# Optimization experiments

Hardware: AMD Instinct MI355X
Metric: run time of the kernel (lower is better)

## Reference

```python
import jax, jax.numpy as jnp
from jax import lax
import numpy as np

B, C, H, W = 64, 3, 224, 224
NPARAM, NSEV, NCHROMA, K = 8, 5, 1, 37
SEVERITY = 3  # ctor default
CHROMA = 0   # random.random()*nchroma made deterministic


def setup_inputs() -> dict:
    key = jax.random.key(0)
    k1, k2, k3, k4, k5 = jax.random.split(key, 5)
    batch = jax.random.uniform(k1, (B, C, H, W), dtype=jnp.float32)
    targets = jax.random.randint(k2, (B,), 0, 1000, dtype=jnp.int32)
    psf_stack = jax.random.uniform(k3, (NPARAM, NSEV, NCHROMA, C, K, K), dtype=jnp.float32)
    params = jax.random.randint(k4, (B,), 0, NPARAM, dtype=jnp.int32)
    weights = jax.random.uniform(k5, (B,), dtype=jnp.float32)
    return {"batch": batch, "targets": targets, "psf_stack": psf_stack,
            "params": params, "weights": weights}


def reference(batch, targets, psf_stack, params, weights):
    # kernels for chosen severity/chroma: [NPARAM, C, K, K]
    kernels = psf_stack[:, SEVERITY - 1, CHROMA]
    k = kernels[params]                      # per-sample kernels [B, C, K, K]
    b, c, h, w = batch.shape
    p = K // 2
    # reflect pad (torch F.pad mode='reflect')
    xp = jnp.pad(batch, ((0, 0), (0, 0), (p, p), (p, p)), mode='reflect')
    # per-sample per-channel (depthwise) conv as one grouped conv with B*C groups
    x = xp.reshape(1, b * c, h + 2 * p, w + 2 * p)
    kw = k.reshape(b * c, 1, K, K)
    blurred = lax.conv_general_dilated(
        x, kw, window_strides=(1, 1), padding='VALID',
        feature_group_count=b * c,
        dimension_numbers=('NCHW', 'OIHW', 'NCHW'),
    ).reshape(b, c, h, w)
    wv = weights.reshape(-1, 1, 1, 1)
    out = (1.0 - wv) * batch + wv * blurred  # normalize is identity by default
    return out, targets
```

## Files before the change

### kernel.cpp

```cpp
#include <hip/hip_runtime.h>

#define BB 64
#define CC 3
#define HH 224
#define WW 224
#define KK 37
#define PP 18
#define PLANE (HH*WW)

#define BM 32
#define BROWS 68
#define BSTR 264
#define FRAGS 2560
#define NTT (8*CC*KK)
#define TT_BYTES ((size_t)NTT * FRAGS * sizeof(unsigned short))

typedef __attribute__((ext_vector_type(8)))  __bf16 bf16x8;
typedef __attribute__((ext_vector_type(4)))  unsigned int u32x4;
typedef __attribute__((ext_vector_type(16))) float  f32x16;

__device__ __forceinline__ unsigned short f2bf(float f) {
    unsigned int u = __float_as_uint(f);
    return (unsigned short)((u + 0x7FFFu + ((u >> 16) & 1u)) >> 16);
}
__device__ __forceinline__ float bf2f(unsigned short h) {
    return __uint_as_float(((unsigned int)h) << 16);
}

__global__ __launch_bounds__(256) void build_frags(
    const float* __restrict__ psf, unsigned short* __restrict__ tt,
    const int* __restrict__ targets, float* __restrict__ tout)
{
    const int s = blockIdx.x;
    const int ky = s % KK;
    const int pc = s / KK;
    const int p = pc / CC, c = pc - (pc / CC) * CC;
    const float* wrow = psf + (size_t)(((p*5 + 2)*CC + c)*KK + ky) * KK;
    unsigned short* dst = tt + (size_t)s * FRAGS;
    for (int e = threadIdx.x; e < FRAGS; e += 256) {
        int j = e & 7, ln = (e >> 3) & 31, hi = (e >> 8) & 1, q = e >> 9;
        int kx = 16*q + 8*hi + j - ln;
        dst[e] = (kx >= 0 && kx < KK) ? f2bf(wrow[kx]) : (unsigned short)0;
    }
    if (s == 0 && threadIdx.x < BB) tout[threadIdx.x] = (float)targets[threadIdx.x];
}

__device__ __forceinline__ void load_bq_asm(u32x4 (&bq)[5], const unsigned short* kybase) {
    const unsigned short* p = kybase + 1024;
    asm volatile("global_load_dwordx4 %0, %1, off offset:-2048" : "=v"(bq[0]) : "v"(p));
    asm volatile("global_load_dwordx4 %0, %1, off offset:-1024" : "=v"(bq[1]) : "v"(p));
    asm volatile("global_load_dwordx4 %0, %1, off"              : "=v"(bq[2]) : "v"(p));
    asm volatile("global_load_dwordx4 %0, %1, off offset:1024"  : "=v"(bq[3]) : "v"(p));
    asm volatile("global_load_dwordx4 %0, %1, off offset:2048"  : "=v"(bq[4]) : "v"(p));
}

__device__ __forceinline__ void load_bq_fb(u32x4 (&bq)[5], const unsigned short* s_w16,
                                           int ky, int hi, int ln) {
    #pragma unroll
    for (int q = 0; q < 5; ++q) {
        union { u32x4 v; unsigned short s[8]; } u;
        #pragma unroll
        for (int j = 0; j < 8; ++j) {
            int kx = 16*q + 8*hi + j - ln;
            u.s[j] = (kx >= 0 && kx < KK) ? s_w16[ky*40 + kx] : (unsigned short)0;
        }
        bq[q] = u.v;
    }
}

#define MFMA_(T,Q) T = __builtin_amdgcn_mfma_f32_32x32x16_bf16( \
    __builtin_bit_cast(bf16x8, af), __builtin_bit_cast(bf16x8, bq[Q]), T, 0, 0, 0)

template<int NT>
__device__ __forceinline__ void compute_ky(const unsigned short* rp, const u32x4 (&bq)[5],
                                           f32x16& A0, f32x16& A1)
{
    u32x4 af;
#define LDC(c) af = *(const u32x4*)(rp + 16*(c))
    if constexpr (NT == 2) {
        LDC(0); MFMA_(A0,0);
        LDC(1); MFMA_(A0,1);
        LDC(2); MFMA_(A0,2); MFMA_(A1,0);
        LDC(3); MFMA_(A0,3); MFMA_(A1,1);
        LDC(4); MFMA_(A0,4); MFMA_(A1,2);
        LDC(5); MFMA_(A1,3);
        LDC(6); MFMA_(A1,4);
    } else {
        LDC(0); MFMA_(A0,0);
        LDC(1); MFMA_(A0,1);
        LDC(2); MFMA_(A0,2);
        LDC(3); MFMA_(A0,3);
        LDC(4); MFMA_(A0,4);
    }
#undef LDC
}

#define SP1 __builtin_amdgcn_s_setprio(1)
#define SP0 __builtin_amdgcn_s_setprio(0)
#define VMWAIT(N) do { asm volatile("s_waitcnt vmcnt(" #N ")" ::: "memory"); \
                       __builtin_amdgcn_sched_barrier(0); } while (0)

template<int NT>
__device__ __forceinline__ void kloop_ws(
    const unsigned short* base, const unsigned short* fb,
    f32x16& A0, f32x16& A1)
{
    u32x4 bqA[5], bqB[5];
    load_bq_asm(bqA, fb);
    load_bq_asm(bqB, fb + FRAGS);
    for (int ky = 0; ky < KK - 2; ky += 2) {
        VMWAIT(5);
        SP1; compute_ky<NT>(base + ky*BSTR, bqA, A0, A1); SP0;
        load_bq_asm(bqA, fb + (size_t)(ky + 2)*FRAGS);
        VMWAIT(5);
        SP1; compute_ky<NT>(base + (ky + 1)*BSTR, bqB, A0, A1); SP0;
        if (ky + 3 < KK)
            load_bq_asm(bqB, fb + (size_t)(ky + 3)*FRAGS);
    }
    VMWAIT(0);
    SP1; compute_ky<NT>(base + (KK - 1)*BSTR, bqA, A0, A1); SP0;
}

template<int NT>
__device__ __forceinline__ void kloop_fb(
    const unsigned short* base, const unsigned short* s_w16,
    int hi, int ln, f32x16& A0, f32x16& A1)
{
    u32x4 bq[5];
    for (int ky = 0; ky < KK; ++ky) {
        load_bq_fb(bq, s_w16, ky, hi, ln);
        compute_ky<NT>(base + ky*BSTR, bq, A0, A1);
    }
}

template<bool FROM_WS>
__global__ __launch_bounds__(256, 4) void optics_mfma(
    const float* __restrict__ batch,
    const float* __restrict__ psf,
    const unsigned short* __restrict__ tt,
    const int* __restrict__ params,
    const float* __restrict__ weights,
    float* __restrict__ out)
{
    __shared__ __align__(16) unsigned short s_band[BROWS*BSTR + 16];
    __shared__ __align__(16) unsigned short s_w16[FROM_WS ? 8 : KK*40];

    const int tid = threadIdx.x;
    const int yband = blockIdx.x;
    const int plane = blockIdx.y;
    const int b = plane / CC, c = plane - b*CC;
    const int y0 = yband * BM;
    const int p = params[b];

    const float* src = batch + (size_t)plane * PLANE;
    for (int i = tid; i < BROWS*56; i += 256) {
        int r = i / 56, g = i - r*56;
        int gy = y0 + r - PP;
        gy = gy < 0 ? -gy : (gy >= HH ? 2*HH - 2 - gy : gy);
        float4 v = *(const float4*)&src[gy*WW + 4*g];
        unsigned int lo  = f2bf(v.x) | ((unsigned int)f2bf(v.y) << 16);
        unsigned int hi2 = f2bf(v.z) | ((unsigned int)f2bf(v.w) << 16);
        unsigned int* d = (unsigned int*)&s_band[r*BSTR + PP + 4*g];
        d[0] = lo; d[1] = hi2;
    }
    for (int i = tid; i < BROWS*40; i += 256) {
        int r = i / 40, e = i - r*40;
        int col = e < PP ? e : (224 + e);
        unsigned short v = 0;
        if (col < 260) {
            int gy = y0 + r - PP;
            gy = gy < 0 ? -gy : (gy >= HH ? 2*HH - 2 - gy : gy);
            int gx = col - PP;
            gx = gx < 0 ? -gx : (gx >= WW ? 2*WW - 2 - gx : gx);
            v = f2bf(src[gy*WW + gx]);
        }
        s_band[r*BSTR + col] = v;
    }
    if (tid < 16) s_band[BROWS*BSTR + tid] = 0;
    if constexpr (!FROM_WS) {
        const float* ksrc = psf + (size_t)((p*5 + 2)*CC + c) * (KK*KK);
        for (int i = tid; i < KK*KK; i += 256) {
            int ky_ = i / KK, kx_ = i - ky_*KK;
            s_w16[ky_*40 + kx_] = f2bf(ksrc[i]);
        }
    }
    __syncthreads();

    const int lane = tid & 63;
    const int w    = tid >> 6;
    const int ln   = lane & 31;
    const int hi   = lane >> 5;

    const unsigned short* base = &s_band[ln*BSTR + 64*w + 8*hi];

    f32x16 A0 = {0,0,0,0, 0,0,0,0, 0,0,0,0, 0,0,0,0};
    f32x16 A1 = A0;

    if constexpr (FROM_WS) {
        const unsigned short* fb = tt + (size_t)((p*CC + c)*KK)*FRAGS + hi*256 + ln*8;
        if (w < 3) kloop_ws<2>(base, fb, A0, A1);
        else       kloop_ws<1>(base, fb, A0, A1);
    } else {
        if (w < 3) kloop_fb<2>(base, s_w16, hi, ln, A0, A1);
        else       kloop_fb<1>(base, s_w16, hi, ln, A0, A1);
    }

    const float wt = weights[b];
    const float w1 = 1.0f - wt;
    float* dst = out + (size_t)plane * PLANE;
#define EPI(ACC, GT) { \
    _Pragma("unroll") \
    for (int r = 0; r < 16; ++r) { \
        const int rowL = (r & 3) + 8*(r >> 2) + 4*hi; \
        const int yo = y0 + rowL; \
        const int xo = 32*(GT) + ln; \
        const float orig = bf2f(s_band[(rowL + PP)*BSTR + xo + PP]); \
        dst[yo*WW + xo] = w1*orig + wt*ACC[r]; \
    } }
    EPI(A0, 2*w)
    if (w < 3) EPI(A1, 2*w + 1)
#undef EPI
}

__global__ void copy_targets(const int* __restrict__ t, float* __restrict__ out) {
    int i = threadIdx.x;
    if (i < BB) out[i] = (float)t[i];
}

extern "C" void kernel_launch(void* const* d_in, const int* in_sizes, int n_in,
                              void* d_out, int out_size, void* d_ws, size_t ws_size,
                              hipStream_t stream) {
    const float* batch   = (const float*)d_in[0];
    const int*   targets = (const int*)d_in[1];
    const float* psf     = (const float*)d_in[2];
    const int*   params  = (const int*)d_in[3];
    const float* weights = (const float*)d_in[4];
    float* out = (float*)d_out;
    unsigned short* tt = (unsigned short*)d_ws;

    dim3 grid(HH / BM, BB*CC);

    if (ws_size >= TT_BYTES) {
        build_frags<<<NTT, 256, 0, stream>>>(psf, tt, targets,
                                             out + (size_t)BB*CC*PLANE);
        optics_mfma<true><<<grid, 256, 0, stream>>>(batch, psf, tt, params, weights, out);
    } else {
        optics_mfma<false><<<grid, 256, 0, stream>>>(batch, psf, tt, params, weights, out);
        copy_targets<<<1, 64, 0, stream>>>(targets, out + (size_t)BB*CC*PLANE);
    }
}
```

Baseline: 78.49 us.

## Enlarge row tile to 64 with 2x2 wave split and swizzled 1D grid

Each block now covers 64 output rows instead of 32, so the 36-row halo is loaded and converted once per 64 rows, and each wave accumulates up to four 32x32 tiles per ky. This cuts halo reload overhead and reuses each B-fragment load across more MFMAs. The grid becomes a 1D launch of 768 blocks whose index is swizzled so neighbouring blocks land on different XCDs. The last band has only 32 rows, so half its waves sit idle. The larger LDS band and extra accumulator registers lower the occupancy target from 4 to 3 blocks per CU.

```diff
diff --git a/kernel.cpp b/kernel.cpp
--- a/kernel.cpp
+++ b/kernel.cpp
@@ -8,12 +8,13 @@
 #define PP 18
 #define PLANE (HH*WW)
 
-#define BM 32
-#define BROWS 68
+#define BM 64
+#define BROWS 100
 #define BSTR 264
 #define FRAGS 2560
 #define NTT (8*CC*KK)
 #define TT_BYTES ((size_t)NTT * FRAGS * sizeof(unsigned short))
+#define NBLK 768
 
 typedef __attribute__((ext_vector_type(8)))  __bf16 bf16x8;
 typedef __attribute__((ext_vector_type(4)))  unsigned int u32x4;
@@ -73,24 +74,26 @@
 
 template<int NT>
 __device__ __forceinline__ void compute_ky(const unsigned short* rp, const u32x4 (&bq)[5],
-                                           f32x16& A0, f32x16& A1)
+                                           f32x16& A0, f32x16& A1, f32x16& A2, f32x16& A3)
 {
     u32x4 af;
 #define LDC(c) af = *(const u32x4*)(rp + 16*(c))
-    if constexpr (NT == 2) {
-        LDC(0); MFMA_(A0,0);
-        LDC(1); MFMA_(A0,1);
-        LDC(2); MFMA_(A0,2); MFMA_(A1,0);
-        LDC(3); MFMA_(A0,3); MFMA_(A1,1);
-        LDC(4); MFMA_(A0,4); MFMA_(A1,2);
-        LDC(5); MFMA_(A1,3);
-        LDC(6); MFMA_(A1,4);
+    LDC(0);  MFMA_(A0,0);
+    LDC(1);  MFMA_(A0,1);
+    LDC(2);  MFMA_(A0,2); MFMA_(A1,0);
+    LDC(3);  MFMA_(A0,3); MFMA_(A1,1);
+    LDC(4);  MFMA_(A0,4); MFMA_(A1,2); MFMA_(A2,0);
+    LDC(5);  MFMA_(A1,3); MFMA_(A2,1);
+    if constexpr (NT == 4) {
+        LDC(6);  MFMA_(A1,4); MFMA_(A2,2); MFMA_(A3,0);
+        LDC(7);  MFMA_(A2,3); MFMA_(A3,1);
+        LDC(8);  MFMA_(A2,4); MFMA_(A3,2);
+        LDC(9);  MFMA_(A3,3);
+        LDC(10); MFMA_(A3,4);
     } else {
-        LDC(0); MFMA_(A0,0);
-        LDC(1); MFMA_(A0,1);
-        LDC(2); MFMA_(A0,2);
-        LDC(3); MFMA_(A0,3);
-        LDC(4); MFMA_(A0,4);
+        LDC(6);  MFMA_(A1,4); MFMA_(A2,2);
+        LDC(7);  MFMA_(A2,3);
+        LDC(8);  MFMA_(A2,4);
     }
 #undef LDC
 }
@@ -103,38 +106,38 @@
 template<int NT>
 __device__ __forceinline__ void kloop_ws(
     const unsigned short* base, const unsigned short* fb,
-    f32x16& A0, f32x16& A1)
+    f32x16& A0, f32x16& A1, f32x16& A2, f32x16& A3)
 {
     u32x4 bqA[5], bqB[5];
     load_bq_asm(bqA, fb);
     load_bq_asm(bqB, fb + FRAGS);
     for (int ky = 0; ky < KK - 2; ky += 2) {
         VMWAIT(5);
-        SP1; compute_ky<NT>(base + ky*BSTR, bqA, A0, A1); SP0;
+        SP1; compute_ky<NT>(base + ky*BSTR, bqA, A0, A1, A2, A3); SP0;
         load_bq_asm(bqA, fb + (size_t)(ky + 2)*FRAGS);
         VMWAIT(5);
-        SP1; compute_ky<NT>(base + (ky + 1)*BSTR, bqB, A0, A1); SP0;
+        SP1; compute_ky<NT>(base + (ky + 1)*BSTR, bqB, A0, A1, A2, A3); SP0;
         if (ky + 3 < KK)
             load_bq_asm(bqB, fb + (size_t)(ky + 3)*FRAGS);
     }
     VMWAIT(0);
-    SP1; compute_ky<NT>(base + (KK - 1)*BSTR, bqA, A0, A1); SP0;
+    SP1; compute_ky<NT>(base + (KK - 1)*BSTR, bqA, A0, A1, A2, A3); SP0;
 }
 
 template<int NT>
 __device__ __forceinline__ void kloop_fb(
     const unsigned short* base, const unsigned short* s_w16,
-    int hi, int ln, f32x16& A0, f32x16& A1)
+    int hi, int ln, f32x16& A0, f32x16& A1, f32x16& A2, f32x16& A3)
 {
     u32x4 bq[5];
     for (int ky = 0; ky < KK; ++ky) {
         load_bq_fb(bq, s_w16, ky, hi, ln);
-        compute_ky<NT>(base + ky*BSTR, bq, A0, A1);
+        compute_ky<NT>(base + ky*BSTR, bq, A0, A1, A2, A3);
     }
 }
 
 template<bool FROM_WS>
-__global__ __launch_bounds__(256, 4) void optics_mfma(
+__global__ __launch_bounds__(256, 3) void optics_mfma(
     const float* __restrict__ batch,
     const float* __restrict__ psf,
     const unsigned short* __restrict__ tt,
@@ -146,14 +149,18 @@
     __shared__ __align__(16) unsigned short s_w16[FROM_WS ? 8 : KK*40];
 
     const int tid = threadIdx.x;
-    const int yband = blockIdx.x;
-    const int plane = blockIdx.y;
+    const int n = blockIdx.x;
+    const int item = (n & 7) * (NBLK / 8) + (n >> 3);
+    const int plane = item >> 2;
+    const int yband = item & 3;
     const int b = plane / CC, c = plane - b*CC;
     const int y0 = yband * BM;
+    const int rows = (HH - y0 < BM) ? (HH - y0) : BM;
+    const int brows = rows + KK - 1;
     const int p = params[b];
 
     const float* src = batch + (size_t)plane * PLANE;
-    for (int i = tid; i < BROWS*56; i += 256) {
+    for (int i = tid; i < brows*56; i += 256) {
         int r = i / 56, g = i - r*56;
         int gy = y0 + r - PP;
         gy = gy < 0 ? -gy : (gy >= HH ? 2*HH - 2 - gy : gy);
@@ -163,7 +170,7 @@
         unsigned int* d = (unsigned int*)&s_band[r*BSTR + PP + 4*g];
         d[0] = lo; d[1] = hi2;
     }
-    for (int i = tid; i < BROWS*40; i += 256) {
+    for (int i = tid; i < brows*40; i += 256) {
         int r = i / 40, e = i - r*40;
         int col = e < PP ? e : (224 + e);
         unsigned short v = 0;
@@ -176,7 +183,7 @@
         }
         s_band[r*BSTR + col] = v;
     }
-    if (tid < 16) s_band[BROWS*BSTR + tid] = 0;
+    if (tid < 16) s_band[brows*BSTR + tid] = 0;
     if constexpr (!FROM_WS) {
         const float* ksrc = psf + (size_t)((p*5 + 2)*CC + c) * (KK*KK);
         for (int i = tid; i < KK*KK; i += 256) {
@@ -187,39 +194,45 @@
     __syncthreads();
 
     const int lane = tid & 63;
-    const int w    = tid >> 6;
+    const int wid  = tid >> 6;
+    const int wr   = wid >> 1;
+    const int xh   = wid & 1;
     const int ln   = lane & 31;
     const int hi   = lane >> 5;
-
-    const unsigned short* base = &s_band[ln*BSTR + 64*w + 8*hi];
-
-    f32x16 A0 = {0,0,0,0, 0,0,0,0, 0,0,0,0, 0,0,0,0};
-    f32x16 A1 = A0;
-
-    if constexpr (FROM_WS) {
-        const unsigned short* fb = tt + (size_t)((p*CC + c)*KK)*FRAGS + hi*256 + ln*8;
-        if (w < 3) kloop_ws<2>(base, fb, A0, A1);
-        else       kloop_ws<1>(base, fb, A0, A1);
+    const bool active = (wr == 0) || (rows > 32);
+
+    if (active) {
+        const unsigned short* base = &s_band[(32*wr + ln)*BSTR + 128*xh + 8*hi];
+
+        f32x16 A0 = {0,0,0,0, 0,0,0,0, 0,0,0,0, 0,0,0,0};
+        f32x16 A1 = A0, A2 = A0, A3 = A0;
+
+        if constexpr (FROM_WS) {
+            const unsigned short* fb = tt + (size_t)((p*CC + c)*KK)*FRAGS + hi*256 + ln*8;
+            if (xh == 0) kloop_ws<4>(base, fb, A0, A1, A2, A3);
+            else         kloop_ws<3>(base, fb, A0, A1, A2, A3);
+        } else {
+            if (xh == 0) kloop_fb<4>(base, s_w16, hi, ln, A0, A1, A2, A3);
+            else         kloop_fb<3>(base, s_w16, hi, ln, A0, A1, A2, A3);
+        }
+
+        const float wt = weights[b];
+        const float w1 = 1.0f - wt;
+        float* dst = out + (size_t)plane * PLANE;
+#define EPI(ACC, GT) { \
+        _Pragma("unroll") \
+        for (int r = 0; r < 16; ++r) { \
+            const int rowL = (r & 3) + 8*(r >> 2) + 4*hi; \
+            const int yo = y0 + 32*wr + rowL; \
+            const int xo = 32*(GT) + ln; \
+            const float orig = bf2f(s_band[(32*wr + rowL + PP)*BSTR + xo + PP]); \
+            dst[yo*WW + xo] = w1*orig + wt*ACC[r]; \
+        } }
+        if (xh == 0) { EPI(A0, 0) EPI(A1, 1) EPI(A2, 2) EPI(A3, 3) }
+        else         { EPI(A0, 4) EPI(A1, 5) EPI(A2, 6) }
+#undef EPI
     } else {
-        if (w < 3) kloop_fb<2>(base, s_w16, hi, ln, A0, A1);
-        else       kloop_fb<1>(base, s_w16, hi, ln, A0, A1);
-    }
-
-    const float wt = weights[b];
-    const float w1 = 1.0f - wt;
-    float* dst = out + (size_t)plane * PLANE;
-#define EPI(ACC, GT) { \
-    _Pragma("unroll") \
-    for (int r = 0; r < 16; ++r) { \
-        const int rowL = (r & 3) + 8*(r >> 2) + 4*hi; \
-        const int yo = y0 + rowL; \
-        const int xo = 32*(GT) + ln; \
-        const float orig = bf2f(s_band[(rowL + PP)*BSTR + xo + PP]); \
-        dst[yo*WW + xo] = w1*orig + wt*ACC[r]; \
-    } }
-    EPI(A0, 2*w)
-    if (w < 3) EPI(A1, 2*w + 1)
-#undef EPI
+    }
 }
 
 __global__ void copy_targets(const int* __restrict__ t, float* __restrict__ out) {
@@ -238,14 +251,12 @@
     float* out = (float*)d_out;
     unsigned short* tt = (unsigned short*)d_ws;
 
-    dim3 grid(HH / BM, BB*CC);
-
     if (ws_size >= TT_BYTES) {
         build_frags<<<NTT, 256, 0, stream>>>(psf, tt, targets,
                                              out + (size_t)BB*CC*PLANE);
-        optics_mfma<true><<<grid, 256, 0, stream>>>(batch, psf, tt, params, weights, out);
+        optics_mfma<true><<<NBLK, 256, 0, stream>>>(batch, psf, tt, params, weights, out);
     } else {
-        optics_mfma<false><<<grid, 256, 0, stream>>>(batch, psf, tt, params, weights, out);
+        optics_mfma<false><<<NBLK, 256, 0, stream>>>(batch, psf, tt, params, weights, out);
         copy_targets<<<1, 64, 0, stream>>>(targets, out + (size_t)BB*CC*PLANE);
     }
 }
```

Result: faster. 68.21 us (-13.1%).

## Double-buffer LDS A-fragment reads alongside weight loads, remap grid blocks

Applied to the files above, without the earlier changes.

Moves the LDS reads of the input-band A fragments into explicit asm ds_read_b128 bursts, issued one ky row ahead into double-buffered registers. They overlap with the prefetched global weight fragments under a combined vmcnt/lgkmcnt wait, so the MFMA clusters no longer stall on per-fragment LDS latency. The 2D grid becomes a 1D grid of 1344 blocks with a strided mapping that interleaves which planes and bands run concurrently, likely to spread L2/XCD locality. Launch bounds drop from 4 to 3 blocks per SIMD group to leave room for the extra registers, at the cost of occupancy.

```diff
diff --git a/kernel.cpp b/kernel.cpp
--- a/kernel.cpp
+++ b/kernel.cpp
@@ -14,10 +14,11 @@
 #define FRAGS 2560
 #define NTT (8*CC*KK)
 #define TT_BYTES ((size_t)NTT * FRAGS * sizeof(unsigned short))
+#define NBLK 1344
 
 typedef __attribute__((ext_vector_type(8)))  __bf16 bf16x8;
 typedef __attribute__((ext_vector_type(4)))  unsigned int u32x4;
-typedef __attribute__((ext_vector_type(16))) float  f32x16;
+typedef __attribute__((ext_vector_type(16))) float f32x16;
 
 __device__ __forceinline__ unsigned short f2bf(float f) {
     unsigned int u = __float_as_uint(f);
@@ -54,6 +55,85 @@
     asm volatile("global_load_dwordx4 %0, %1, off offset:2048"  : "=v"(bq[4]) : "v"(p));
 }
 
+template<int NC>
+__device__ __forceinline__ void ds_burst(u32x4 (&af)[NC], const unsigned short* rp) {
+    unsigned a = (unsigned)(uintptr_t)rp;
+    asm volatile("ds_read_b128 %0, %1 offset:0"   : "=v"(af[0]) : "v"(a));
+    asm volatile("ds_read_b128 %0, %1 offset:32"  : "=v"(af[1]) : "v"(a));
+    asm volatile("ds_read_b128 %0, %1 offset:64"  : "=v"(af[2]) : "v"(a));
+    asm volatile("ds_read_b128 %0, %1 offset:96"  : "=v"(af[3]) : "v"(a));
+    asm volatile("ds_read_b128 %0, %1 offset:128" : "=v"(af[4]) : "v"(a));
+    if constexpr (NC > 5) {
+        asm volatile("ds_read_b128 %0, %1 offset:160" : "=v"(af[5]) : "v"(a));
+        asm volatile("ds_read_b128 %0, %1 offset:192" : "=v"(af[6]) : "v"(a));
+    }
+}
+
+template<int NC>
+__device__ __forceinline__ void wait_both() {
+    if constexpr (NC == 7)
+        asm volatile("s_waitcnt vmcnt(5) lgkmcnt(7)" ::: "memory");
+    else
+        asm volatile("s_waitcnt vmcnt(5) lgkmcnt(5)" ::: "memory");
+    __builtin_amdgcn_sched_barrier(0);
+}
+
+#define MFMA_(T,AF,Q) T = __builtin_amdgcn_mfma_f32_32x32x16_bf16( \
+    __builtin_bit_cast(bf16x8, af[AF]), __builtin_bit_cast(bf16x8, bq[Q]), T, 0, 0, 0)
+
+template<int NT, int NC>
+__device__ __forceinline__ void cluster(const u32x4 (&af)[NC], const u32x4 (&bq)[5],
+                                        f32x16& A0, f32x16& A1)
+{
+    if constexpr (NT == 2) {
+        MFMA_(A0,0,0);
+        MFMA_(A0,1,1);
+        MFMA_(A0,2,2); MFMA_(A1,2,0);
+        MFMA_(A0,3,3); MFMA_(A1,3,1);
+        MFMA_(A0,4,4); MFMA_(A1,4,2);
+        MFMA_(A1,5,3);
+        MFMA_(A1,6,4);
+    } else {
+        MFMA_(A0,0,0);
+        MFMA_(A0,1,1);
+        MFMA_(A0,2,2);
+        MFMA_(A0,3,3);
+        MFMA_(A0,4,4);
+    }
+}
+
+#define SP1 __builtin_amdgcn_s_setprio(1)
+#define SP0 __builtin_amdgcn_s_setprio(0)
+
+template<int NT>
+__device__ __forceinline__ void kloop_ws(
+    const unsigned short* base,
+    const unsigned short* fb,
+    f32x16& A0, f32x16& A1)
+{
+    constexpr int NC = (NT == 2) ? 7 : 5;
+    u32x4 afA[NC], afB[NC], bqA[5], bqB[5];
+    ds_burst<NC>(afA, base);
+    load_bq_asm(bqA, fb);
+    ds_burst<NC>(afB, base + BSTR);
+    load_bq_asm(bqB, fb + FRAGS);
+    for (int ky = 0; ky < KK - 2; ky += 2) {
+        wait_both<NC>();
+        SP1; cluster<NT, NC>(afA, bqA, A0, A1); SP0;
+        ds_burst<NC>(afA, base + (ky + 2)*BSTR);
+        load_bq_asm(bqA, fb + (size_t)(ky + 2)*FRAGS);
+        wait_both<NC>();
+        SP1; cluster<NT, NC>(afB, bqB, A0, A1); SP0;
+        if (ky + 3 < KK) {
+            ds_burst<NC>(afB, base + (ky + 3)*BSTR);
+            load_bq_asm(bqB, fb + (size_t)(ky + 3)*FRAGS);
+        }
+    }
+    asm volatile("s_waitcnt vmcnt(0) lgkmcnt(0)" ::: "memory");
+    __builtin_amdgcn_sched_barrier(0);
+    SP1; cluster<NT, NC>(afA, bqA, A0, A1); SP0;
+}
+
 __device__ __forceinline__ void load_bq_fb(u32x4 (&bq)[5], const unsigned short* s_w16,
                                            int ky, int hi, int ln) {
     #pragma unroll
@@ -68,73 +148,23 @@
     }
 }
 
-#define MFMA_(T,Q) T = __builtin_amdgcn_mfma_f32_32x32x16_bf16( \
-    __builtin_bit_cast(bf16x8, af), __builtin_bit_cast(bf16x8, bq[Q]), T, 0, 0, 0)
-
-template<int NT>
-__device__ __forceinline__ void compute_ky(const unsigned short* rp, const u32x4 (&bq)[5],
-                                           f32x16& A0, f32x16& A1)
-{
-    u32x4 af;
-#define LDC(c) af = *(const u32x4*)(rp + 16*(c))
-    if constexpr (NT == 2) {
-        LDC(0); MFMA_(A0,0);
-        LDC(1); MFMA_(A0,1);
-        LDC(2); MFMA_(A0,2); MFMA_(A1,0);
-        LDC(3); MFMA_(A0,3); MFMA_(A1,1);
-        LDC(4); MFMA_(A0,4); MFMA_(A1,2);
-        LDC(5); MFMA_(A1,3);
-        LDC(6); MFMA_(A1,4);
-    } else {
-        LDC(0); MFMA_(A0,0);
-        LDC(1); MFMA_(A0,1);
-        LDC(2); MFMA_(A0,2);
-        LDC(3); MFMA_(A0,3);
-        LDC(4); MFMA_(A0,4);
-    }
-#undef LDC
-}
-
-#define SP1 __builtin_amdgcn_s_setprio(1)
-#define SP0 __builtin_amdgcn_s_setprio(0)
-#define VMWAIT(N) do { asm volatile("s_waitcnt vmcnt(" #N ")" ::: "memory"); \
-                       __builtin_amdgcn_sched_barrier(0); } while (0)
-
-template<int NT>
-__device__ __forceinline__ void kloop_ws(
-    const unsigned short* base, const unsigned short* fb,
-    f32x16& A0, f32x16& A1)
-{
-    u32x4 bqA[5], bqB[5];
-    load_bq_asm(bqA, fb);
-    load_bq_asm(bqB, fb + FRAGS);
-    for (int ky = 0; ky < KK - 2; ky += 2) {
-        VMWAIT(5);
-        SP1; compute_ky<NT>(base + ky*BSTR, bqA, A0, A1); SP0;
-        load_bq_asm(bqA, fb + (size_t)(ky + 2)*FRAGS);
-        VMWAIT(5);
-        SP1; compute_ky<NT>(base + (ky + 1)*BSTR, bqB, A0, A1); SP0;
-        if (ky + 3 < KK)
-            load_bq_asm(bqB, fb + (size_t)(ky + 3)*FRAGS);
-    }
-    VMWAIT(0);
-    SP1; compute_ky<NT>(base + (KK - 1)*BSTR, bqA, A0, A1); SP0;
-}
-
-template<int NT>
+template<int NT, int NC>
 __device__ __forceinline__ void kloop_fb(
     const unsigned short* base, const unsigned short* s_w16,
     int hi, int ln, f32x16& A0, f32x16& A1)
 {
-    u32x4 bq[5];
+    u32x4 af[NC], bq[5];
     for (int ky = 0; ky < KK; ++ky) {
         load_bq_fb(bq, s_w16, ky, hi, ln);
-        compute_ky<NT>(base + ky*BSTR, bq, A0, A1);
+        #pragma unroll
+        for (int c = 0; c < NC; ++c)
+            af[c] = *(const u32x4*)(base + ky*BSTR + 16*c);
+        cluster<NT, NC>(af, bq, A0, A1);
     }
 }
 
 template<bool FROM_WS>
-__global__ __launch_bounds__(256, 4) void optics_mfma(
+__global__ __launch_bounds__(256, 3) void optics_mfma(
     const float* __restrict__ batch,
     const float* __restrict__ psf,
     const unsigned short* __restrict__ tt,
@@ -146,8 +176,10 @@
     __shared__ __align__(16) unsigned short s_w16[FROM_WS ? 8 : KK*40];
 
     const int tid = threadIdx.x;
-    const int yband = blockIdx.x;
-    const int plane = blockIdx.y;
+    const int n = blockIdx.x;
+    const int item = (n & 7) * (NBLK / 8) + (n >> 3);
+    const int plane = item / 7;
+    const int yband = item - plane*7;
     const int b = plane / CC, c = plane - b*CC;
     const int y0 = yband * BM;
     const int p = params[b];
@@ -201,8 +233,8 @@
         if (w < 3) kloop_ws<2>(base, fb, A0, A1);
         else       kloop_ws<1>(base, fb, A0, A1);
     } else {
-        if (w < 3) kloop_fb<2>(base, s_w16, hi, ln, A0, A1);
-        else       kloop_fb<1>(base, s_w16, hi, ln, A0, A1);
+        if (w < 3) kloop_fb<2, 7>(base, s_w16, hi, ln, A0, A1);
+        else       kloop_fb<1, 5>(base, s_w16, hi, ln, A0, A1);
     }
 
     const float wt = weights[b];
@@ -238,14 +270,12 @@
     float* out = (float*)d_out;
     unsigned short* tt = (unsigned short*)d_ws;
 
-    dim3 grid(HH / BM, BB*CC);
-
     if (ws_size >= TT_BYTES) {
         build_frags<<<NTT, 256, 0, stream>>>(psf, tt, targets,
                                              out + (size_t)BB*CC*PLANE);
-        optics_mfma<true><<<grid, 256, 0, stream>>>(batch, psf, tt, params, weights, out);
+        optics_mfma<true><<<NBLK, 256, 0, stream>>>(batch, psf, tt, params, weights, out);
     } else {
-        optics_mfma<false><<<grid, 256, 0, stream>>>(batch, psf, tt, params, weights, out);
+        optics_mfma<false><<<NBLK, 256, 0, stream>>>(batch, psf, tt, params, weights, out);
         copy_targets<<<1, 64, 0, stream>>>(targets, out + (size_t)BB*CC*PLANE);
     }
 }
```

New measurement: 79.52 us. Within noise of the previous version (+1.3%).
